# Optimization experiments

Measured on AMD Instinct MI355X. Metric: run time of the kernel, lower is better.

Reference implementation:

```python
import jax, jax.numpy as jnp
import numpy as np

N_NODES = 100000
N_EDGES = 1600000
IN_CH = 128
NHIDDEN = 64
OUT_CH = 40
NLAYERS = 4
ALPHA = 0.1


def setup_inputs() -> dict:
    key = jax.random.key(0)
    ks = jax.random.split(key, 7)
    x = jax.random.normal(ks[0], (N_NODES, IN_CH), dtype=jnp.float32)
    edge_index = jax.random.randint(ks[1], (2, N_EDGES), 0, N_NODES, dtype=jnp.int64)
    batch_graph = jnp.zeros((N_NODES,), dtype=jnp.int64)
    fc1_w = jax.random.normal(ks[2], (NHIDDEN, IN_CH), dtype=jnp.float32) * (1.0 / np.sqrt(IN_CH))
    fc1_b = jax.random.normal(ks[3], (NHIDDEN,), dtype=jnp.float32) * 0.01
    conv_w = jax.random.normal(ks[4], (NLAYERS, NHIDDEN, NHIDDEN), dtype=jnp.float32) * (1.0 / np.sqrt(NHIDDEN))
    fc2_w = jax.random.normal(ks[5], (OUT_CH, NHIDDEN), dtype=jnp.float32) * (1.0 / np.sqrt(NHIDDEN))
    fc2_b = jax.random.normal(ks[6], (OUT_CH,), dtype=jnp.float32) * 0.01
    return {"x": x, "edge_index": edge_index, "batch_graph": batch_graph,
            "fc1_w": fc1_w, "fc1_b": fc1_b, "conv_w": conv_w,
            "fc2_w": fc2_w, "fc2_b": fc2_b}


def reference(x, edge_index, batch_graph, fc1_w, fc1_b, conv_w, fc2_w, fc2_b):
    # eval mode: dropout layers are identity
    n = x.shape[0]
    row, col = edge_index[0], edge_index[1]  # source, target

    # gcn_norm with add_self_loops=False: sym deg^-1/2 normalization
    deg = jax.ops.segment_sum(jnp.ones_like(row, dtype=x.dtype), col, num_segments=n)
    dinv = jnp.where(deg > 0, deg ** -0.5, 0.0)
    norm = (dinv[row] * dinv[col])[:, None]  # [E, 1]

    h = jax.nn.relu(x @ fc1_w.T + fc1_b)  # [N, nhidden]
    h0 = h
    nlayers = conv_w.shape[0]
    for i in range(nlayers):
        # GCN2Conv: aggregate, initial-residual mix, weight1 matmul (beta=1)
        agg = jax.ops.segment_sum(h[row] * norm, col, num_segments=n)
        mixed = (1.0 - ALPHA) * agg + ALPHA * h0
        h = jax.nn.relu(mixed @ conv_w[i])
    out = h @ fc2_w.T + fc2_b  # [N, out_channels]
    return out
```

## Files before the change

### kernel.cpp

```cpp
#include <hip/hip_runtime.h>
#include <hip/hip_fp16.h>

#define N_NODES 100000
#define N_EDGES 1600000
#define IN_CH   128
#define NHID    64
#define OUT_CH  40
#define NBLK    391
#define NBUCK   196
#define BCAP    8960
#define ECAP    1024


__global__ __launch_bounds__(256) void k_scan1(const int* __restrict__ cnt,
                                               int* __restrict__ rowptr,
                                               int* __restrict__ bsum) {
    __shared__ int s[256];
    int t = threadIdx.x;
    int n = blockIdx.x * 256 + t;
    int v = (n < N_NODES) ? cnt[n] : 0;
    s[t] = v;
    __syncthreads();
    for (int off = 1; off < 256; off <<= 1) {
        int add = (t >= off) ? s[t - off] : 0;
        __syncthreads();
        s[t] += add;
        __syncthreads();
    }
    int incl = s[t];
    if (n < N_NODES) rowptr[n] = incl - v;
    if (t == 255) bsum[blockIdx.x] = incl;
}

__global__ __launch_bounds__(512) void k_scan2(int* __restrict__ bsum) {
    __shared__ int s[512];
    int t = threadIdx.x;
    int v = (t < NBLK) ? bsum[t] : 0;
    s[t] = v;
    __syncthreads();
    for (int off = 1; off < 512; off <<= 1) {
        int add = (t >= off) ? s[t - off] : 0;
        __syncthreads();
        s[t] += add;
        __syncthreads();
    }
    if (t < NBLK) bsum[t] = s[t] - v;
}

__global__ __launch_bounds__(256) void k_scan3(const int* __restrict__ cnt,
                                               const int* __restrict__ bsum,
                                               int* __restrict__ rowptr,
                                               float* __restrict__ dinv) {
    int n = blockIdx.x * 256 + threadIdx.x;
    if (n < N_NODES) {
        int rp = rowptr[n] + bsum[n >> 8];
        rowptr[n] = rp;
        int c = cnt[n];
        dinv[n] = (c > 0) ? rsqrtf((float)c) : 0.0f;
    }
    if (blockIdx.x == 0 && threadIdx.x == 0) rowptr[N_NODES] = N_EDGES;
}


__global__ __launch_bounds__(256) void k_scatA(const int* __restrict__ ei,
                                               int* __restrict__ bucketCnt,
                                               int2* __restrict__ ebufA) {
    __shared__ int hist[NBUCK];
    __shared__ int base[NBUCK];
    int t = threadIdx.x;
    int chunk = blockIdx.x * 4096;
    for (int i = t; i < NBUCK; i += 256) hist[i] = 0;
    __syncthreads();
#pragma unroll 4
    for (int i = 0; i < 16; i++) {
        int e = chunk + i * 256 + t;
        if (e < N_EDGES) atomicAdd(&hist[ei[N_EDGES + e] >> 9], 1);
    }
    __syncthreads();
    for (int b = t; b < NBUCK; b += 256) {
        int h = hist[b];
        base[b] = h ? atomicAdd(&bucketCnt[b], h) : 0;
    }
    __syncthreads();
#pragma unroll 4
    for (int i = 0; i < 16; i++) {
        int e = chunk + i * 256 + t;
        if (e < N_EDGES) {
            int r = ei[e], c = ei[N_EDGES + e];
            int pos = atomicAdd(&base[c >> 9], 1);
            ebufA[(size_t)(c >> 9) * BCAP + pos] = make_int2(r, c);
        }
    }
}


__global__ __launch_bounds__(256) void k_deg(const int2* __restrict__ ebufA,
                                             const int* __restrict__ bucketCnt,
                                             int* __restrict__ cnt) {
    __shared__ int hist[512];
    int b = blockIdx.x;
    int nodeB = b * 512;
    int t = threadIdx.x;
    for (int i = t; i < 512; i += 256) hist[i] = 0;
    __syncthreads();
    int nE = bucketCnt[b];
    const int2* src = ebufA + (size_t)b * BCAP;
    for (int i = t; i < nE; i += 256) atomicAdd(&hist[src[i].y - nodeB], 1);
    __syncthreads();
    for (int i = t; i < 512; i += 256) {
        int node = nodeB + i;
        if (node < N_NODES) cnt[node] = hist[i];
    }
}


__global__ __launch_bounds__(256) void k_scatB(const int2* __restrict__ ebufA,
                                               const int* __restrict__ bucketCnt,
                                               const float* __restrict__ dinv,
                                               const int* __restrict__ rowptr,
                                               int2* __restrict__ e8) {
    __shared__ int lcur[512];
    int b = blockIdx.x;
    int nodeB = b * 512;
    int t = threadIdx.x;
    for (int i = t; i < 512; i += 256) {
        int node = nodeB + i;
        lcur[i] = (node < N_NODES) ? rowptr[node] : 0;
    }
    __syncthreads();
    int nE = bucketCnt[b];
    const int2* src = ebufA + (size_t)b * BCAP;
    for (int i = t; i < nE; i += 256) {
        int2 rc = src[i];
        float w = dinv[rc.x] * dinv[rc.y];
        int pos = atomicAdd(&lcur[rc.y - nodeB], 1);
        e8[pos] = make_int2(rc.x, __float_as_int(w));
    }
}

__device__ __forceinline__ void store_h4(__half* dst, float a, float b, float c, float d) {
    union { uint2 u; __half2 h[2]; } pk;
    pk.h[0] = __floats2half2_rn(a, b);
    pk.h[1] = __floats2half2_rn(c, d);
    *(uint2*)dst = pk.u;
}


__global__ __launch_bounds__(256, 4) void k_fc1(const float* __restrict__ x,
                                                const float* __restrict__ w,
                                                const float* __restrict__ b,
                                                float* __restrict__ h0,
                                                __half* __restrict__ h016) {
    __shared__ float xs[64 * 128];
    int t = threadIdx.x;
    int nodeBase = blockIdx.x * 64;

    {
        int nl = t >> 2, seg = t & 3;
        int n = nodeBase + nl;
        int swz = (nl ^ (nl >> 3)) & 7;
        float4* dstrow = (float4*)(xs + nl * 128);
        if (n < N_NODES) {
            const float4* src = (const float4*)(x + (size_t)n * IN_CH + seg * 32);
#pragma unroll
            for (int q = 0; q < 8; q++) dstrow[(seg * 8 + q) ^ swz] = src[q];
        } else {
            float4 z = {0.f, 0.f, 0.f, 0.f};
#pragma unroll
            for (int q = 0; q < 8; q++) dstrow[(seg * 8 + q) ^ swz] = z;
        }
    }
    __syncthreads();

    int tx = t & 15, ty = t >> 4;
    int n0 = tx * 4, o0 = ty * 4;
    int swz0 = ((n0 + 0) ^ ((n0 + 0) >> 3)) & 7;
    int swz1 = ((n0 + 1) ^ ((n0 + 1) >> 3)) & 7;
    int swz2 = ((n0 + 2) ^ ((n0 + 2) >> 3)) & 7;
    int swz3 = ((n0 + 3) ^ ((n0 + 3) >> 3)) & 7;
    const float4* xrow0 = (const float4*)(xs + (n0 + 0) * 128);
    const float4* xrow1 = (const float4*)(xs + (n0 + 1) * 128);
    const float4* xrow2 = (const float4*)(xs + (n0 + 2) * 128);
    const float4* xrow3 = (const float4*)(xs + (n0 + 3) * 128);

    float c[4][4];
#pragma unroll
    for (int i = 0; i < 4; i++)
#pragma unroll
        for (int j = 0; j < 4; j++) c[i][j] = 0.f;

#pragma unroll 4
    for (int k = 0; k < IN_CH; k += 4) {
        int kk = k >> 2;
        float4 b0 = *(const float4*)&w[(size_t)(o0 + 0) * IN_CH + k];
        float4 b1 = *(const float4*)&w[(size_t)(o0 + 1) * IN_CH + k];
        float4 b2 = *(const float4*)&w[(size_t)(o0 + 2) * IN_CH + k];
        float4 b3 = *(const float4*)&w[(size_t)(o0 + 3) * IN_CH + k];
        float4 a0 = xrow0[kk ^ swz0];
        float4 a1 = xrow1[kk ^ swz1];
        float4 a2 = xrow2[kk ^ swz2];
        float4 a3 = xrow3[kk ^ swz3];
#pragma unroll
        for (int i = 0; i < 4; i++) {
            float4 a = (i == 0) ? a0 : (i == 1) ? a1 : (i == 2) ? a2 : a3;
            c[i][0] = fmaf(a.x, b0.x, fmaf(a.y, b0.y, fmaf(a.z, b0.z, fmaf(a.w, b0.w, c[i][0]))));
            c[i][1] = fmaf(a.x, b1.x, fmaf(a.y, b1.y, fmaf(a.z, b1.z, fmaf(a.w, b1.w, c[i][1]))));
            c[i][2] = fmaf(a.x, b2.x, fmaf(a.y, b2.y, fmaf(a.z, b2.z, fmaf(a.w, b2.w, c[i][2]))));
            c[i][3] = fmaf(a.x, b3.x, fmaf(a.y, b3.y, fmaf(a.z, b3.z, fmaf(a.w, b3.w, c[i][3]))));
        }
    }

    float4 bias = *(const float4*)&b[o0];
#pragma unroll
    for (int i = 0; i < 4; i++) {
        int n = nodeBase + n0 + i;
        if (n < N_NODES) {
            float4 v;
            v.x = fmaxf(c[i][0] + bias.x, 0.f);
            v.y = fmaxf(c[i][1] + bias.y, 0.f);
            v.z = fmaxf(c[i][2] + bias.z, 0.f);
            v.w = fmaxf(c[i][3] + bias.w, 0.f);
            *(float4*)&h0[(size_t)n * NHID + o0] = v;
            store_h4(&h016[(size_t)n * NHID + o0], v.x, v.y, v.z, v.w);
        }
    }
}


__global__ __launch_bounds__(256, 4) void k_conv(const __half* __restrict__ hin,
                                                 const float* __restrict__ h0,
                                                 const int* __restrict__ rowptr,
                                                 const int2* __restrict__ e8,
                                                 const float* __restrict__ W,
                                                 __half* __restrict__ hout) {
    __shared__ int2  eS[ECAP];
    __shared__ float mix[32 * 68];
    int t = threadIdx.x;
    int nodeBase = blockIdx.x * 32;
    int grp = t >> 3;
    int cg = (t & 7) * 8;

    int base0 = rowptr[nodeBase];
    int nE = rowptr[nodeBase + 32] - base0;
    int nStage = (nE < ECAP) ? nE : ECAP;
    for (int i = t; i < nStage; i += 256) eS[i] = e8[base0 + i];

    int n = nodeBase + grp;
    int s = rowptr[n], e = rowptr[n + 1];
    int d = e - s;
    int hi = (d > 0) ? (e - 1) : 0;
    __syncthreads();

    float acc[8];
#pragma unroll
    for (int i = 0; i < 8; i++) acc[i] = 0.f;

#define LOADM(pm, jb)                                                    \
    {                                                                    \
        _Pragma("unroll")                                                \
        for (int u = 0; u < 4; u++) {                                    \
            int idx = min((jb) + u, hi);                                 \
            int li = idx - base0;                                        \
            if (li < ECAP) pm[u] = eS[li];                               \
            else           pm[u] = e8[idx];                              \
        }                                                                \
    }
#define ISSUE(pv, pm)                                                    \
    {                                                                    \
        _Pragma("unroll")                                                \
        for (int u = 0; u < 4; u++)                                      \
            pv[u] = *(const float4*)&hin[(size_t)pm[u].x * NHID + cg];   \
    }
#define FMA4(cm, cv, jb)                                                 \
    {                                                                    \
        _Pragma("unroll")                                                \
        for (int u = 0; u < 4; u++) {                                    \
            float wgt = ((jb) + u < e) ? __int_as_float(cm[u].y) : 0.f;  \
            const __half2* hp = (const __half2*)&cv[u];                  \
            _Pragma("unroll")                                            \
            for (int q = 0; q < 4; q++) {                                \
                float2 f = __half22float2(hp[q]);                        \
                acc[q * 2 + 0] = fmaf(wgt, f.x, acc[q * 2 + 0]);         \
                acc[q * 2 + 1] = fmaf(wgt, f.y, acc[q * 2 + 1]);         \
            }                                                            \
        }                                                                \
    }

    int2  pmA[4], pmB[4];
    float4 pvA[4], pvB[4];
    if (d > 0) {
        LOADM(pmA, s);     ISSUE(pvA, pmA);
        LOADM(pmB, s + 4); ISSUE(pvB, pmB);
    }

    for (int j = s; j < e; j += 8) {
        {
            int2 cm[4]; float4 cv[4];
#pragma unroll
            for (int u = 0; u < 4; u++) { cm[u] = pmA[u]; cv[u] = pvA[u]; }
            int jn = j + 8;
            if (jn < e) { LOADM(pmA, jn); ISSUE(pvA, pmA); }
            FMA4(cm, cv, j);
        }
        if (j + 4 < e) {
            int2 cm[4]; float4 cv[4];
#pragma unroll
            for (int u = 0; u < 4; u++) { cm[u] = pmB[u]; cv[u] = pvB[u]; }
            int jn = j + 12;
            if (jn < e) { LOADM(pmB, jn); ISSUE(pvB, pmB); }
            FMA4(cm, cv, j + 4);
        }
    }
#undef LOADM
#undef ISSUE
#undef FMA4

    {
        float4 h0a = *(const float4*)&h0[(size_t)n * NHID + cg];
        float4 h0b = *(const float4*)&h0[(size_t)n * NHID + cg + 4];
        float4 m0, m1;
        m0.x = fmaf(0.9f, acc[0], 0.1f * h0a.x);
        m0.y = fmaf(0.9f, acc[1], 0.1f * h0a.y);
        m0.z = fmaf(0.9f, acc[2], 0.1f * h0a.z);
        m0.w = fmaf(0.9f, acc[3], 0.1f * h0a.w);
        m1.x = fmaf(0.9f, acc[4], 0.1f * h0b.x);
        m1.y = fmaf(0.9f, acc[5], 0.1f * h0b.y);
        m1.z = fmaf(0.9f, acc[6], 0.1f * h0b.z);
        m1.w = fmaf(0.9f, acc[7], 0.1f * h0b.w);
        *(float4*)&mix[grp * 68 + cg] = m0;
        *(float4*)&mix[grp * 68 + cg + 4] = m1;
    }
    __syncthreads();

    int tx = t & 15, ty = t >> 4;
    int o0 = tx * 4, r0 = ty * 2;
    float c[2][4];
#pragma unroll
    for (int i = 0; i < 2; i++)
#pragma unroll
        for (int j = 0; j < 4; j++) c[i][j] = 0.f;

#pragma unroll 4
    for (int k = 0; k < NHID; k += 4) {
        float4 b0 = *(const float4*)&W[(k + 0) * NHID + o0];
        float4 b1 = *(const float4*)&W[(k + 1) * NHID + o0];
        float4 b2 = *(const float4*)&W[(k + 2) * NHID + o0];
        float4 b3 = *(const float4*)&W[(k + 3) * NHID + o0];
#pragma unroll
        for (int i = 0; i < 2; i++) {
            float4 a = *(const float4*)&mix[(r0 + i) * 68 + k];
            c[i][0] = fmaf(a.x, b0.x, fmaf(a.y, b1.x, fmaf(a.z, b2.x, fmaf(a.w, b3.x, c[i][0]))));
            c[i][1] = fmaf(a.x, b0.y, fmaf(a.y, b1.y, fmaf(a.z, b2.y, fmaf(a.w, b3.y, c[i][1]))));
            c[i][2] = fmaf(a.x, b0.z, fmaf(a.y, b1.z, fmaf(a.z, b2.z, fmaf(a.w, b3.z, c[i][2]))));
            c[i][3] = fmaf(a.x, b0.w, fmaf(a.y, b1.w, fmaf(a.z, b2.w, fmaf(a.w, b3.w, c[i][3]))));
        }
    }
#pragma unroll
    for (int i = 0; i < 2; i++) {
        int n2 = nodeBase + r0 + i;
        store_h4(&hout[(size_t)n2 * NHID + o0],
                 fmaxf(c[i][0], 0.f), fmaxf(c[i][1], 0.f),
                 fmaxf(c[i][2], 0.f), fmaxf(c[i][3], 0.f));
    }
}


__global__ __launch_bounds__(256) void k_fc2(const __half* __restrict__ h,
                                             const float* __restrict__ w,
                                             const float* __restrict__ b,
                                             float* __restrict__ out) {
    __shared__ float wT[NHID * 44];
    __shared__ float hs[64 * 68];
    int t = threadIdx.x;
    int nodeBase = blockIdx.x * 64;

    for (int id = t; id < NHID * OUT_CH; id += 256) {
        int o = id >> 6, k = id & 63;
        wT[k * 44 + o] = w[id];
    }
    {
        int nl = t >> 2, seg = t & 3;
        int n = nodeBase + nl;
        float* dst = hs + nl * 68 + seg * 16;
        if (n < N_NODES) {
            float4 raw0 = *(const float4*)&h[(size_t)n * NHID + seg * 16];
            float4 raw1 = *(const float4*)&h[(size_t)n * NHID + seg * 16 + 8];
            const __half2* hp0 = (const __half2*)&raw0;
            const __half2* hp1 = (const __half2*)&raw1;
#pragma unroll
            for (int q = 0; q < 4; q++) {
                float2 f = __half22float2(hp0[q]);
                dst[q * 2 + 0] = f.x;
                dst[q * 2 + 1] = f.y;
            }
#pragma unroll
            for (int q = 0; q < 4; q++) {
                float2 f = __half22float2(hp1[q]);
                dst[8 + q * 2 + 0] = f.x;
                dst[8 + q * 2 + 1] = f.y;
            }
        } else {
#pragma unroll
            for (int q = 0; q < 16; q++) dst[q] = 0.f;
        }
    }
    __syncthreads();

    if (t < 160) {
        int tx = t % 10, ty = t / 10;
        int o0 = tx * 4, n0 = ty * 4;
        float c[4][4];
#pragma unroll
        for (int i = 0; i < 4; i++)
#pragma unroll
            for (int j = 0; j < 4; j++) c[i][j] = 0.f;

#pragma unroll 4
        for (int k = 0; k < NHID; k += 4) {
            float4 b0 = *(const float4*)&wT[(k + 0) * 44 + o0];
            float4 b1 = *(const float4*)&wT[(k + 1) * 44 + o0];
            float4 b2 = *(const float4*)&wT[(k + 2) * 44 + o0];
            float4 b3 = *(const float4*)&wT[(k + 3) * 44 + o0];
#pragma unroll
            for (int i = 0; i < 4; i++) {
                float4 a = *(const float4*)&hs[(n0 + i) * 68 + k];
                c[i][0] = fmaf(a.x, b0.x, fmaf(a.y, b1.x, fmaf(a.z, b2.x, fmaf(a.w, b3.x, c[i][0]))));
                c[i][1] = fmaf(a.x, b0.y, fmaf(a.y, b1.y, fmaf(a.z, b2.y, fmaf(a.w, b3.y, c[i][1]))));
                c[i][2] = fmaf(a.x, b0.z, fmaf(a.y, b1.z, fmaf(a.z, b2.z, fmaf(a.w, b3.z, c[i][2]))));
                c[i][3] = fmaf(a.x, b0.w, fmaf(a.y, b1.w, fmaf(a.z, b2.w, fmaf(a.w, b3.w, c[i][3]))));
            }
        }
        float4 bias = *(const float4*)&b[o0];
#pragma unroll
        for (int i = 0; i < 4; i++) {
            int n = nodeBase + n0 + i;
            if (n < N_NODES) {
                float4 v;
                v.x = c[i][0] + bias.x;
                v.y = c[i][1] + bias.y;
                v.z = c[i][2] + bias.z;
                v.w = c[i][3] + bias.w;
                *(float4*)&out[(size_t)n * OUT_CH + o0] = v;
            }
        }
    }
}


extern "C" void kernel_launch(void* const* d_in, const int* in_sizes, int n_in,
                              void* d_out, int out_size, void* d_ws, size_t ws_size,
                              hipStream_t stream) {
    const float* x    = (const float*)d_in[0];
    const int*   ei   = (const int*)d_in[1];
    const float* fc1w = (const float*)d_in[3];
    const float* fc1b = (const float*)d_in[4];
    const float* cw   = (const float*)d_in[5];
    const float* fc2w = (const float*)d_in[6];
    const float* fc2b = (const float*)d_in[7];
    float* out = (float*)d_out;

    char* p = (char*)d_ws;
    auto alloc = [&](size_t bytes) { char* r = p; p += (bytes + 255) & ~(size_t)255; return r; };
    float*  h0     = (float*) alloc((size_t)N_NODES * NHID * 4);
    __half* h016   = (__half*)alloc((size_t)N_NODES * NHID * 2);
    __half* ha16   = (__half*)alloc((size_t)N_NODES * NHID * 2);
    __half* hb16   = (__half*)alloc((size_t)N_NODES * NHID * 2);
    int2*   e8     = (int2*)  alloc(((size_t)N_EDGES + 8) * 8);
    int2*   ebufA  = (int2*)  alloc((size_t)NBUCK * BCAP * 8);
    int*    cnt    = (int*)   alloc((size_t)N_NODES * 4);
    int*    rowptr = (int*)   alloc((size_t)(N_NODES + 1) * 4);
    int*    bCnt   = (int*)   alloc((size_t)NBUCK * 4);
    float*  dinv   = (float*) alloc((size_t)N_NODES * 4);
    int*    bsum   = (int*)   alloc(512 * 4);

    hipMemsetAsync(bCnt, 0, (size_t)NBUCK * 4, stream);
    k_scatA<<<(N_EDGES + 4095) / 4096, 256, 0, stream>>>(ei, bCnt, ebufA);
    k_deg  <<<NBUCK, 256, 0, stream>>>(ebufA, bCnt, cnt);
    k_scan1<<<NBLK, 256, 0, stream>>>(cnt, rowptr, bsum);
    k_scan2<<<1, 512, 0, stream>>>(bsum);
    k_scan3<<<NBLK, 256, 0, stream>>>(cnt, bsum, rowptr, dinv);
    k_scatB<<<NBUCK, 256, 0, stream>>>(ebufA, bCnt, dinv, rowptr, e8);

    int gb64 = (N_NODES + 63) / 64;
    int gb32 = N_NODES / 32;
    k_fc1 <<<gb64, 256, 0, stream>>>(x, fc1w, fc1b, h0, h016);
    k_conv<<<gb32, 256, 0, stream>>>(h016, h0, rowptr, e8, cw + 0 * NHID * NHID, ha16);
    k_conv<<<gb32, 256, 0, stream>>>(ha16, h0, rowptr, e8, cw + 1 * NHID * NHID, hb16);
    k_conv<<<gb32, 256, 0, stream>>>(hb16, h0, rowptr, e8, cw + 2 * NHID * NHID, ha16);
    k_conv<<<gb32, 256, 0, stream>>>(ha16, h0, rowptr, e8, cw + 3 * NHID * NHID, hb16);
    k_fc2 <<<gb64, 256, 0, stream>>>(hb16, fc2w, fc2b, out);
}
```

Baseline: 425.8 us.

## Drop fp32 h0 copy, deepen gather prefetch to three stages, coalesce fc1 loads

The fp32 copy of h0 is removed, and the initial-residual term in each conv layer now reads the fp16 h016 buffer. This cuts fc1 write traffic and halves per-layer h0 reads, at some precision cost in the residual mix. The conv edge gather moves from two in-flight prefetch groups to three (12 edges in flight) to hide more gather latency, which costs extra registers. The fc1 x tile load is also remapped so consecutive lanes read consecutive float4s, for better coalescing.

```diff
diff --git a/kernel.cpp b/kernel.cpp
--- a/kernel.cpp
+++ b/kernel.cpp
@@ -149,25 +149,28 @@
 __global__ __launch_bounds__(256, 4) void k_fc1(const float* __restrict__ x,
                                                 const float* __restrict__ w,
                                                 const float* __restrict__ b,
-                                                float* __restrict__ h0,
                                                 __half* __restrict__ h016) {
     __shared__ float xs[64 * 128];
     int t = threadIdx.x;
     int nodeBase = blockIdx.x * 64;
 
     {
-        int nl = t >> 2, seg = t & 3;
-        int n = nodeBase + nl;
-        int swz = (nl ^ (nl >> 3)) & 7;
-        float4* dstrow = (float4*)(xs + nl * 128);
-        if (n < N_NODES) {
-            const float4* src = (const float4*)(x + (size_t)n * IN_CH + seg * 32);
-#pragma unroll
-            for (int q = 0; q < 8; q++) dstrow[(seg * 8 + q) ^ swz] = src[q];
-        } else {
-            float4 z = {0.f, 0.f, 0.f, 0.f};
-#pragma unroll
-            for (int q = 0; q < 8; q++) dstrow[(seg * 8 + q) ^ swz] = z;
+        int lane8 = t & 7, rhalf = t >> 3;
+#pragma unroll
+        for (int r2 = 0; r2 < 2; r2++) {
+            int nl = r2 * 32 + rhalf;
+            int n = nodeBase + nl;
+            int swz = (nl ^ (nl >> 3)) & 7;
+            float4* dstrow = (float4*)(xs + nl * 128);
+            if (n < N_NODES) {
+                const float4* src = (const float4*)(x + (size_t)n * IN_CH);
+#pragma unroll
+                for (int q = 0; q < 4; q++) dstrow[(q * 8 + lane8) ^ swz] = src[q * 8 + lane8];
+            } else {
+                float4 z = {0.f, 0.f, 0.f, 0.f};
+#pragma unroll
+                for (int q = 0; q < 4; q++) dstrow[(q * 8 + lane8) ^ swz] = z;
+            }
         }
     }
     __syncthreads();
@@ -215,20 +218,16 @@
     for (int i = 0; i < 4; i++) {
         int n = nodeBase + n0 + i;
         if (n < N_NODES) {
-            float4 v;
-            v.x = fmaxf(c[i][0] + bias.x, 0.f);
-            v.y = fmaxf(c[i][1] + bias.y, 0.f);
-            v.z = fmaxf(c[i][2] + bias.z, 0.f);
-            v.w = fmaxf(c[i][3] + bias.w, 0.f);
-            *(float4*)&h0[(size_t)n * NHID + o0] = v;
-            store_h4(&h016[(size_t)n * NHID + o0], v.x, v.y, v.z, v.w);
+            store_h4(&h016[(size_t)n * NHID + o0],
+                     fmaxf(c[i][0] + bias.x, 0.f), fmaxf(c[i][1] + bias.y, 0.f),
+                     fmaxf(c[i][2] + bias.z, 0.f), fmaxf(c[i][3] + bias.w, 0.f));
         }
     }
 }
 
 
 __global__ __launch_bounds__(256, 4) void k_conv(const __half* __restrict__ hin,
-                                                 const float* __restrict__ h0,
+                                                 const __half* __restrict__ h0f16,
                                                  const int* __restrict__ rowptr,
                                                  const int2* __restrict__ e8,
                                                  const float* __restrict__ W,
@@ -271,44 +270,41 @@
         for (int u = 0; u < 4; u++)                                      \
             pv[u] = *(const float4*)&hin[(size_t)pm[u].x * NHID + cg];   \
     }
-#define FMA4(cm, cv, jb)                                                 \
+#define FMA4(pm, pv, jb)                                                 \
     {                                                                    \
         _Pragma("unroll")                                                \
         for (int u = 0; u < 4; u++) {                                    \
-            float wgt = ((jb) + u < e) ? __int_as_float(cm[u].y) : 0.f;  \
-            const __half2* hp = (const __half2*)&cv[u];                  \
+            float wgt = ((jb) + u < e) ? __int_as_float(pm[u].y) : 0.f;  \
+            const __half* hp = (const __half*)&pv[u];                    \
             _Pragma("unroll")                                            \
-            for (int q = 0; q < 4; q++) {                                \
-                float2 f = __half22float2(hp[q]);                        \
-                acc[q * 2 + 0] = fmaf(wgt, f.x, acc[q * 2 + 0]);         \
-                acc[q * 2 + 1] = fmaf(wgt, f.y, acc[q * 2 + 1]);         \
-            }                                                            \
+            for (int q = 0; q < 8; q++)                                  \
+                acc[q] = fmaf(wgt, __half2float(hp[q]), acc[q]);         \
         }                                                                \
     }
 
-    int2  pmA[4], pmB[4];
-    float4 pvA[4], pvB[4];
+    int2  pmA[4], pmB[4], pmC[4];
+    float4 pvA[4], pvB[4], pvC[4];
     if (d > 0) {
         LOADM(pmA, s);     ISSUE(pvA, pmA);
         LOADM(pmB, s + 4); ISSUE(pvB, pmB);
-    }
-
-    for (int j = s; j < e; j += 8) {
+        LOADM(pmC, s + 8); ISSUE(pvC, pmC);
+    }
+
+    for (int j = s; j < e; j += 12) {
         {
-            int2 cm[4]; float4 cv[4];
-#pragma unroll
-            for (int u = 0; u < 4; u++) { cm[u] = pmA[u]; cv[u] = pvA[u]; }
-            int jn = j + 8;
+            FMA4(pmA, pvA, j);
+            int jn = j + 12;
             if (jn < e) { LOADM(pmA, jn); ISSUE(pvA, pmA); }
-            FMA4(cm, cv, j);
         }
         if (j + 4 < e) {
-            int2 cm[4]; float4 cv[4];
-#pragma unroll
-            for (int u = 0; u < 4; u++) { cm[u] = pmB[u]; cv[u] = pvB[u]; }
-            int jn = j + 12;
+            FMA4(pmB, pvB, j + 4);
+            int jn = j + 16;
             if (jn < e) { LOADM(pmB, jn); ISSUE(pvB, pmB); }
-            FMA4(cm, cv, j + 4);
+        }
+        if (j + 8 < e) {
+            FMA4(pmC, pvC, j + 8);
+            int jn = j + 20;
+            if (jn < e) { LOADM(pmC, jn); ISSUE(pvC, pmC); }
         }
     }
 #undef LOADM
@@ -316,17 +312,14 @@
 #undef FMA4
 
     {
-        float4 h0a = *(const float4*)&h0[(size_t)n * NHID + cg];
-        float4 h0b = *(const float4*)&h0[(size_t)n * NHID + cg + 4];
-        float4 m0, m1;
-        m0.x = fmaf(0.9f, acc[0], 0.1f * h0a.x);
-        m0.y = fmaf(0.9f, acc[1], 0.1f * h0a.y);
-        m0.z = fmaf(0.9f, acc[2], 0.1f * h0a.z);
-        m0.w = fmaf(0.9f, acc[3], 0.1f * h0a.w);
-        m1.x = fmaf(0.9f, acc[4], 0.1f * h0b.x);
-        m1.y = fmaf(0.9f, acc[5], 0.1f * h0b.y);
-        m1.z = fmaf(0.9f, acc[6], 0.1f * h0b.z);
-        m1.w = fmaf(0.9f, acc[7], 0.1f * h0b.w);
+        float4 raw = *(const float4*)&h0f16[(size_t)n * NHID + cg];
+        const __half* h0h = (const __half*)&raw;
+        float m[8];
+#pragma unroll
+        for (int q = 0; q < 8; q++)
+            m[q] = fmaf(0.9f, acc[q], 0.1f * __half2float(h0h[q]));
+        float4 m0 = {m[0], m[1], m[2], m[3]};
+        float4 m1 = {m[4], m[5], m[6], m[7]};
         *(float4*)&mix[grp * 68 + cg] = m0;
         *(float4*)&mix[grp * 68 + cg + 4] = m1;
     }
@@ -461,7 +454,6 @@
 
     char* p = (char*)d_ws;
     auto alloc = [&](size_t bytes) { char* r = p; p += (bytes + 255) & ~(size_t)255; return r; };
-    float*  h0     = (float*) alloc((size_t)N_NODES * NHID * 4);
     __half* h016   = (__half*)alloc((size_t)N_NODES * NHID * 2);
     __half* ha16   = (__half*)alloc((size_t)N_NODES * NHID * 2);
     __half* hb16   = (__half*)alloc((size_t)N_NODES * NHID * 2);
@@ -483,10 +475,10 @@
 
     int gb64 = (N_NODES + 63) / 64;
     int gb32 = N_NODES / 32;
-    k_fc1 <<<gb64, 256, 0, stream>>>(x, fc1w, fc1b, h0, h016);
-    k_conv<<<gb32, 256, 0, stream>>>(h016, h0, rowptr, e8, cw + 0 * NHID * NHID, ha16);
-    k_conv<<<gb32, 256, 0, stream>>>(ha16, h0, rowptr, e8, cw + 1 * NHID * NHID, hb16);
-    k_conv<<<gb32, 256, 0, stream>>>(hb16, h0, rowptr, e8, cw + 2 * NHID * NHID, ha16);
-    k_conv<<<gb32, 256, 0, stream>>>(ha16, h0, rowptr, e8, cw + 3 * NHID * NHID, hb16);
+    k_fc1 <<<gb64, 256, 0, stream>>>(x, fc1w, fc1b, h016);
+    k_conv<<<gb32, 256, 0, stream>>>(h016, h016, rowptr, e8, cw + 0 * NHID * NHID, ha16);
+    k_conv<<<gb32, 256, 0, stream>>>(ha16, h016, rowptr, e8, cw + 1 * NHID * NHID, hb16);
+    k_conv<<<gb32, 256, 0, stream>>>(hb16, h016, rowptr, e8, cw + 2 * NHID * NHID, ha16);
+    k_conv<<<gb32, 256, 0, stream>>>(ha16, h016, rowptr, e8, cw + 3 * NHID * NHID, hb16);
     k_fc2 <<<gb64, 256, 0, stream>>>(hb16, fc2w, fc2b, out);
 }
```

New measurement: 425.1 us. Within noise of the previous version (-0.2%).
